# Kernel optimization log

Hardware: AMD Instinct MI355X
Metric: run time of the kernel (lower is better)

Reference implementation:

```python
import jax, jax.numpy as jnp
import numpy as np

EPS = 1e-12  # F.normalize eps

def _l2norm(x, axis=-1):
    n = jnp.sqrt(jnp.sum(x * x, axis=axis, keepdims=True))
    return x / jnp.maximum(n, EPS)

def setup_inputs() -> dict:
    key = jax.random.key(0)
    k1, k2, k3, k4 = jax.random.split(key, 4)
    B, S, L, E, H = 16, 4096, 512, 1024, 1024
    return {
        'input_data': jax.random.normal(k1, (B, S, H), dtype=jnp.float32),
        'label_repr': jax.random.normal(k2, (B, L, E), dtype=jnp.float32),
        'W_proj': jax.random.normal(k3, (H, E), dtype=jnp.float32) * (1.0 / np.sqrt(E)),
        'padding_mask': jax.random.randint(k4, (B, S), 0, 2, dtype=jnp.int32),
    }

def reference(input_data, label_repr, W_proj, padding_mask):
    # project labels: [B, L, E] @ [E, H] -> [B, L, H]
    lab = jnp.einsum('ble,he->blh', label_repr, W_proj)
    x_n = _l2norm(input_data, axis=-1)        # [B, S, H]
    lab_n = _l2norm(lab, axis=-1)             # [B, L, H] (== normalize dim=1 after transpose)
    G = jnp.einsum('bsh,blh->bsl', x_n, lab_n)  # cosine scores [B, S, L]
    mask = (padding_mask == 0)[:, :, None]    # True where padded
    G = jnp.where(mask, -jnp.inf, G)
    softmax_G = jax.nn.softmax(G, axis=1)     # softmax over sequence axis
    output = jnp.einsum('bsl,bsh->blh', softmax_G, x_n)  # [B, L, H]
    return (output, softmax_G)
```

## Files before the change

kernel.cpp:

```cpp
#include <hip/hip_runtime.h>
#include <hip/hip_bf16.h>
#include <cmath>

#define B_DIM 16
#define S_DIM 4096
#define L_DIM 512
#define E_DIM 1024
#define H_DIM 1024

typedef __bf16 bf16;
typedef __attribute__((ext_vector_type(8))) __bf16 bf16x8;
typedef __attribute__((ext_vector_type(4))) __bf16 bf16x4;
typedef __attribute__((ext_vector_type(4))) float f32x4;
typedef __attribute__((ext_vector_type(8))) unsigned short u16x8;

__device__ __forceinline__ void gload_lds16(const void* g, void* l) {
  __builtin_amdgcn_global_load_lds((const __attribute__((address_space(1))) void*)g,
                                   (__attribute__((address_space(3))) void*)l,
                                   16, 0, 0);
}

#define SWZ(o) ((o) ^ ((((o) >> 9) & 1) << 5))

__global__ void k_cast(const float* __restrict__ in, bf16* __restrict__ out, int n4) {
  int stride = gridDim.x * blockDim.x;
  for (int i = blockIdx.x * blockDim.x + threadIdx.x; i < n4; i += stride) {
    float4 v = reinterpret_cast<const float4*>(in)[i];
    bf16x4 o = { (bf16)v.x, (bf16)v.y, (bf16)v.z, (bf16)v.w };
    reinterpret_cast<bf16x4*>(out)[i] = o;
  }
}

__global__ __launch_bounds__(256) void k_rownorm_f32(const float* __restrict__ in,
                                                     bf16* __restrict__ out, int nrows) {
  const int wave = (blockIdx.x * 256 + threadIdx.x) >> 6;
  const int lane = threadIdx.x & 63;
  const int nw = (gridDim.x * 256) >> 6;
  for (int r = wave; r < nrows; r += nw) {
    const float4* src = reinterpret_cast<const float4*>(in + (size_t)r * 1024);
    float4 v[4];
    float ss = 0.f;
#pragma unroll
    for (int j = 0; j < 4; ++j) {
      v[j] = src[lane + j * 64];
      ss += v[j].x * v[j].x + v[j].y * v[j].y + v[j].z * v[j].z + v[j].w * v[j].w;
    }
#pragma unroll
    for (int off = 32; off; off >>= 1) ss += __shfl_xor(ss, off);
    const float inv = 1.0f / fmaxf(sqrtf(ss), 1e-12f);
    bf16x4* dst = reinterpret_cast<bf16x4*>(out + (size_t)r * 1024);
#pragma unroll
    for (int j = 0; j < 4; ++j) {
      bf16x4 o = { (bf16)(v[j].x * inv), (bf16)(v[j].y * inv), (bf16)(v[j].z * inv),
                   (bf16)(v[j].w * inv) };
      dst[lane + j * 64] = o;
    }
  }
}

__global__ __launch_bounds__(256) void k_rownorm_add(const float* __restrict__ P,
                                                     bf16* __restrict__ out, int nrows) {
  const int wave = (blockIdx.x * 256 + threadIdx.x) >> 6;
  const int lane = threadIdx.x & 63;
  const int nw = (gridDim.x * 256) >> 6;
  for (int r = wave; r < nrows; r += nw) {
    const int b = r >> 9, l = r & 511;
    const float* p0 = P + ((size_t)b * 1024 + l) * 1024;
    const float4* s0 = reinterpret_cast<const float4*>(p0);
    const float4* s1 = reinterpret_cast<const float4*>(p0 + 524288);
    float4 v[4];
    float ss = 0.f;
#pragma unroll
    for (int j = 0; j < 4; ++j) {
      float4 a = s0[lane + j * 64], c = s1[lane + j * 64];
      v[j] = make_float4(a.x + c.x, a.y + c.y, a.z + c.z, a.w + c.w);
      ss += v[j].x * v[j].x + v[j].y * v[j].y + v[j].z * v[j].z + v[j].w * v[j].w;
    }
#pragma unroll
    for (int off = 32; off; off >>= 1) ss += __shfl_xor(ss, off);
    const float inv = 1.0f / fmaxf(sqrtf(ss), 1e-12f);
    bf16x4* dst = reinterpret_cast<bf16x4*>(out + (size_t)r * 1024);
#pragma unroll
    for (int j = 0; j < 4; ++j) {
      bf16x4 o = { (bf16)(v[j].x * inv), (bf16)(v[j].y * inv), (bf16)(v[j].z * inv),
                   (bf16)(v[j].w * inv) };
      dst[lane + j * 64] = o;
    }
  }
}

__global__ void k_addout(const float* __restrict__ P, float* __restrict__ out, int total4,
                         int LH4) {
  int stride = gridDim.x * blockDim.x;
  for (int i = blockIdx.x * blockDim.x + threadIdx.x; i < total4; i += stride) {
    int b = i / LH4, rem = i - b * LH4;
    const float4* p0 = reinterpret_cast<const float4*>(P) + (size_t)b * 2 * LH4 + rem;
    float4 a = p0[0], c = p0[LH4];
    reinterpret_cast<float4*>(out)[i] = make_float4(a.x + c.x, a.y + c.y, a.z + c.z, a.w + c.w);
  }
}

__global__ __launch_bounds__(256) void k_transpose(const bf16* __restrict__ in,
                                                   bf16* __restrict__ out, int R, int C) {
  __shared__ unsigned short tile[64][72];
  const int r0 = blockIdx.x * 64, c0 = blockIdx.y * 64;
  const size_t boff = (size_t)blockIdx.z * (size_t)R * C;
  const unsigned short* src = (const unsigned short*)in + boff;
  unsigned short* dst = (unsigned short*)out + boff;
  const int t = threadIdx.x;
#pragma unroll
  for (int p = 0; p < 2; ++p) {
    int r = p * 32 + (t >> 3);
    int c = (t & 7) * 8;
    u16x8 v = *reinterpret_cast<const u16x8*>(src + (size_t)(r0 + r) * C + c0 + c);
#pragma unroll
    for (int j = 0; j < 8; ++j) tile[r][c + j] = v[j];
  }
  __syncthreads();
#pragma unroll
  for (int p = 0; p < 2; ++p) {
    int cc = p * 32 + (t >> 3);
    int rr = (t & 7) * 8;
    u16x8 o;
#pragma unroll
    for (int j = 0; j < 8; ++j) o[j] = tile[rr + j][cc];
    *reinterpret_cast<u16x8*>(dst + (size_t)(c0 + cc) * R + r0 + rr) = o;
  }
}

template <int MODE, int KSPLIT>
__global__ __launch_bounds__(512, 2) void k_gemm8(
    const bf16* __restrict__ Aall, const bf16* __restrict__ Ball, void* __restrict__ Call,
    const int N, const int ldk, const int Klen, const size_t sA, const size_t sB,
    const size_t sC, const int lg_nbx, const int* __restrict__ mask,
    float2* __restrict__ part) {
  extern __shared__ char lds[];
  const int bid = blockIdx.x, ntot = gridDim.x;
  const int wg = (bid & 7) * (ntot >> 3) + (bid >> 3);
  const int by = wg & 1;
  const int tmp2 = wg >> 1;
  const int bx = tmp2 & ((1 << lg_nbx) - 1);
  const int z = tmp2 >> lg_nbx;
  const int b = z / KSPLIT, ks = z - b * KSPLIT;
  const int koff = ks * Klen;
  const int t = threadIdx.x, wid = t >> 6, lane = t & 63;
  const int wm = wid >> 2, wn = wid & 3;
  const int lane_r = lane & 15;
  const int lane_k = (lane >> 4) * 16;
  const int row0 = by * 256, col0 = bx * 256;
  const bf16* srcA = Aall + (size_t)b * sA + (size_t)row0 * ldk + koff;
  const bf16* srcB = Ball + (size_t)b * sB + (size_t)col0 * ldk + koff;
  const int NKT = Klen >> 6;

  int s_r[2], s_ce[2];
#pragma unroll
  for (int li = 0; li < 2; ++li) {
    int o = li * 8192 + t * 16;
    int so = SWZ(o);
    s_r[li] = so >> 7;
    s_ce[li] = (so & 127) >> 1;
  }

  f32x4 acc[8][4];
#pragma unroll
  for (int i = 0; i < 8; ++i)
#pragma unroll
    for (int j = 0; j < 4; ++j) acc[i][j] = (f32x4){0.f, 0.f, 0.f, 0.f};

  bf16x8 aq[4][2], b0[2][2], b1[2][2];

  auto STAGE = [&](int c, int isB, int h, const bf16* src, int kt_idx) {
#pragma unroll
    for (int li = 0; li < 2; ++li) {
      const bf16* g = src + (size_t)(h * 128 + s_r[li]) * ldk + (kt_idx * 64 + s_ce[li]);
      char* d = lds + c * 65536 + isB * 32768 + h * 16384 + li * 8192 + wid * 1024;
      gload_lds16(g, d);
    }
  };
  auto LDA = [&](int c, int mh) {
#pragma unroll
    for (int mi = 0; mi < 4; ++mi)
#pragma unroll
      for (int kk = 0; kk < 2; ++kk) {
        int rl = (mh * 4 + mi) * 16 + lane_r;
        int o = rl * 128 + lane_k + kk * 64;
        aq[mi][kk] =
            *reinterpret_cast<const bf16x8*>(lds + c * 65536 + wm * 16384 + SWZ(o));
      }
  };
  auto LDB = [&](int c, int nh, bf16x8(&bq)[2][2]) {
#pragma unroll
    for (int ni = 0; ni < 2; ++ni)
#pragma unroll
      for (int kk = 0; kk < 2; ++kk) {
        int rl = (wn & 1) * 64 + (nh * 2 + ni) * 16 + lane_r;
        int o = rl * 128 + lane_k + kk * 64;
        bq[ni][kk] = *reinterpret_cast<const bf16x8*>(lds + c * 65536 + 32768 +
                                                      (wn >> 1) * 16384 + SWZ(o));
      }
  };
  auto MMA = [&](int mh, int nh, bf16x8(&bq)[2][2]) {
#pragma unroll
    for (int mi = 0; mi < 4; ++mi)
#pragma unroll
      for (int ni = 0; ni < 2; ++ni)
#pragma unroll
        for (int kk = 0; kk < 2; ++kk)
          acc[mh * 4 + mi][nh * 2 + ni] = __builtin_amdgcn_mfma_f32_16x16x32_bf16(
              aq[mi][kk], bq[ni][kk], acc[mh * 4 + mi][nh * 2 + ni], 0, 0, 0);
  };

#define GS_BEGIN                                        \
  __builtin_amdgcn_s_barrier();                         \
  asm volatile("s_waitcnt lgkmcnt(0)" ::: "memory");    \
  __builtin_amdgcn_sched_barrier(0);                    \
  __builtin_amdgcn_s_setprio(1);
#define GS_END                                          \
  __builtin_amdgcn_s_setprio(0);                        \
  __builtin_amdgcn_s_barrier();

  STAGE(0, 0, 0, srcA, 0);
  STAGE(0, 1, 0, srcB, 0);
  STAGE(0, 0, 1, srcA, 0);
  STAGE(0, 1, 1, srcB, 0);
  STAGE(1, 0, 0, srcA, 1);
  STAGE(1, 1, 0, srcB, 1);
  STAGE(1, 0, 1, srcA, 1);
  asm volatile("s_waitcnt vmcnt(6)" ::: "memory");
  __builtin_amdgcn_s_barrier();

#pragma unroll 1
  for (int kt = 0; kt < NKT; kt += 2) {
    const bool s2 = kt + 2 < NKT, s3 = kt + 3 < NKT;
    LDA(0, 0);
    LDB(0, 0, b0);
    STAGE(1, 1, 1, srcB, kt + 1);
    GS_BEGIN; MMA(0, 0, b0); GS_END;
    LDB(0, 1, b1);
    GS_BEGIN; MMA(0, 1, b1); GS_END;
    LDA(0, 1);
    if (s2) STAGE(0, 1, 0, srcB, kt + 2);
    GS_BEGIN; MMA(1, 1, b1); GS_END;
    if (s2) {
      STAGE(0, 0, 0, srcA, kt + 2);
      asm volatile("s_waitcnt vmcnt(4)" ::: "memory");
    } else {
      asm volatile("s_waitcnt vmcnt(0)" ::: "memory");
    }
    GS_BEGIN; MMA(1, 0, b0); GS_END;
    LDA(1, 0);
    LDB(1, 0, b0);
    if (s2) STAGE(0, 1, 1, srcB, kt + 2);
    GS_BEGIN; MMA(0, 0, b0); GS_END;
    LDB(1, 1, b1);
    if (s2) STAGE(0, 0, 1, srcA, kt + 2);
    GS_BEGIN; MMA(0, 1, b1); GS_END;
    LDA(1, 1);
    if (s3) STAGE(1, 1, 0, srcB, kt + 3);
    GS_BEGIN; MMA(1, 1, b1); GS_END;
    if (s3) {
      STAGE(1, 0, 0, srcA, kt + 3);
      STAGE(1, 0, 1, srcA, kt + 3);
      asm volatile("s_waitcnt vmcnt(6)" ::: "memory");
    } else {
      asm volatile("s_waitcnt vmcnt(0)" ::: "memory");
    }
    GS_BEGIN; MMA(1, 0, b0); GS_END;
  }
#undef GS_BEGIN
#undef GS_END

  const int rb = row0 + wm * 128 + (lane >> 4) * 4;
  const int cb = col0 + wn * 64 + lane_r;
  if (MODE == 2) {
    bf16* C = (bf16*)Call + (size_t)z * sC;
#pragma unroll
    for (int mf = 0; mf < 8; ++mf)
#pragma unroll
      for (int nf = 0; nf < 4; ++nf)
#pragma unroll
        for (int r = 0; r < 4; ++r)
          C[(size_t)(rb + mf * 16 + r) * N + cb + nf * 16] = (bf16)acc[mf][nf][r];
    bool vld[4];
#pragma unroll
    for (int nf = 0; nf < 4; ++nf)
      vld[nf] = mask[(size_t)b * N + col0 + wn * 64 + nf * 16 + lane_r] != 0;
    float2* smb = reinterpret_cast<float2*>(lds);
#pragma unroll
    for (int mf = 0; mf < 8; ++mf)
#pragma unroll
      for (int r = 0; r < 4; ++r) {
        float m = -INFINITY;
#pragma unroll
        for (int nf = 0; nf < 4; ++nf)
          if (vld[nf]) m = fmaxf(m, acc[mf][nf][r]);
#pragma unroll
        for (int off = 1; off < 16; off <<= 1) m = fmaxf(m, __shfl_xor(m, off));
        float zz = 0.f;
#pragma unroll
        for (int nf = 0; nf < 4; ++nf)
          if (vld[nf]) zz += __expf(acc[mf][nf][r] - m);
#pragma unroll
        for (int off = 1; off < 16; off <<= 1) zz += __shfl_xor(zz, off);
        if (lane_r == 0)
          smb[(wm * 128 + mf * 16 + (lane >> 4) * 4 + r) * 4 + wn] = make_float2(m, zz);
      }
    __syncthreads();
    if (t < 256) {
      float2 p0 = smb[t * 4 + 0], p1 = smb[t * 4 + 1], p2 = smb[t * 4 + 2],
             p3 = smb[t * 4 + 3];
      float M = fmaxf(fmaxf(p0.x, p1.x), fmaxf(p2.x, p3.x));
      float Z = 0.f;
      if (M != -INFINITY)
        Z = p0.y * __expf(p0.x - M) + p1.y * __expf(p1.x - M) + p2.y * __expf(p2.x - M) +
            p3.y * __expf(p3.x - M);
      part[((size_t)b * L_DIM + row0 + t) * 16 + bx] = make_float2(M, Z);
    }
  } else {
    float* C = (float*)Call + (size_t)z * sC;
#pragma unroll
    for (int mf = 0; mf < 8; ++mf)
#pragma unroll
      for (int nf = 0; nf < 4; ++nf)
#pragma unroll
        for (int r = 0; r < 4; ++r)
          C[(size_t)(rb + mf * 16 + r) * N + cb + nf * 16] = acc[mf][nf][r];
  }
}

__global__ void k_sm_comb(const float2* __restrict__ part, float2* __restrict__ mz, int n) {
  int id = blockIdx.x * blockDim.x + threadIdx.x;
  if (id >= n) return;
  float2 p[16];
  float M = -INFINITY;
#pragma unroll
  for (int q = 0; q < 16; ++q) {
    p[q] = part[(size_t)id * 16 + q];
    M = fmaxf(M, p[q].x);
  }
  float Z = 0.f;
  if (M != -INFINITY) {
#pragma unroll
    for (int q = 0; q < 16; ++q)
      if (p[q].x != -INFINITY) Z += p[q].y * __expf(p[q].x - M);
  }
  float rZ = (Z > 0.f) ? 1.0f / Z : 0.f;
  mz[id] = make_float2(M, rZ);
}

__global__ __launch_bounds__(256) void k_sm_write(bf16* __restrict__ GT,
                                                  const int* __restrict__ mask,
                                                  const float2* __restrict__ mz,
                                                  float* __restrict__ out1) {
  __shared__ float tile[64][65];
  const int b = blockIdx.z, lt = blockIdx.y, sc = blockIdx.x;
  const int t = threadIdx.x, w = t >> 6, lane = t & 63;
  const int s_base = sc * 512;
  for (int st = 0; st < 8; ++st) {
    const int s_tile = s_base + st * 64;
    const bool v = (mask[(size_t)b * S_DIM + s_tile + lane] != 0);
#pragma unroll
    for (int i = 0; i < 16; ++i) {
      const int l = lt * 64 + w * 16 + i;
      const float2 mzv = mz[(size_t)b * L_DIM + l];
      bf16* rp = GT + ((size_t)b * L_DIM + l) * S_DIM + s_tile + lane;
      const float g = (float)*rp;
      const float p = (v && mzv.x != -INFINITY) ? __expf(g - mzv.x) * mzv.y : 0.f;
      *rp = (bf16)p;
      tile[lane][w * 16 + i] = p;
    }
    __syncthreads();
#pragma unroll
    for (int q = 0; q < 16; ++q) {
      const int s_local = q * 4 + w;
      out1[((size_t)b * S_DIM + s_tile + s_local) * L_DIM + lt * 64 + lane] =
          tile[s_local][lane];
    }
    __syncthreads();
  }
}

extern "C" void kernel_launch(void* const* d_in, const int* in_sizes, int n_in, void* d_out,
                              int out_size, void* d_ws, size_t ws_size, hipStream_t stream) {
  const float* input_data = (const float*)d_in[0];
  const float* label_repr = (const float*)d_in[1];
  const float* W_proj = (const float*)d_in[2];
  const int* padding = (const int*)d_in[3];
  float* out0 = (float*)d_out;
  float* out1 = out0 + (size_t)B_DIM * L_DIM * H_DIM;

  char* ws = (char*)d_ws;
  bf16* xn = (bf16*)(ws + 0);
  bf16* xnT = (bf16*)(ws + 134217728);
  bf16* labb = (bf16*)(ws + 268435456);
  bf16* Wb = (bf16*)(ws + 285212672);
  bf16* lab = (bf16*)(ws + 287309824);
  bf16* GT = (bf16*)(ws + 304087040);
  float2* part = (float2*)(ws + 371195904);
  float2* mz = (float2*)(ws + 372244480);
  float* Pk2 = (float*)(ws + 304087040);
  float* Pk5 = (float*)(ws + 0);

  (void)hipFuncSetAttribute((const void*)k_gemm8<0, 2>,
                            hipFuncAttributeMaxDynamicSharedMemorySize, 131072);
  (void)hipFuncSetAttribute((const void*)k_gemm8<2, 1>,
                            hipFuncAttributeMaxDynamicSharedMemorySize, 131072);

  k_cast<<<2048, 256, 0, stream>>>(label_repr, labb, (B_DIM * L_DIM * E_DIM) / 4);
  k_cast<<<512, 256, 0, stream>>>(W_proj, Wb, (H_DIM * E_DIM) / 4);
  k_rownorm_f32<<<2048, 256, 0, stream>>>(input_data, xn, B_DIM * S_DIM);
  k_transpose<<<dim3(S_DIM / 64, H_DIM / 64, B_DIM), 256, 0, stream>>>(xn, xnT, S_DIM, H_DIM);
  k_gemm8<0, 2><<<256, 512, 131072, stream>>>(labb, Wb, Pk2, H_DIM, E_DIM, 512,
                                              (size_t)L_DIM * E_DIM, 0,
                                              (size_t)L_DIM * H_DIM, 2, nullptr, nullptr);
  k_rownorm_add<<<512, 256, 0, stream>>>(Pk2, lab, B_DIM * L_DIM);
  k_gemm8<2, 1><<<512, 512, 131072, stream>>>(lab, xn, GT, S_DIM, H_DIM, H_DIM,
                                              (size_t)L_DIM * H_DIM, (size_t)S_DIM * H_DIM,
                                              (size_t)L_DIM * S_DIM, 4, padding, part);
  k_sm_comb<<<(B_DIM * L_DIM + 255) / 256, 256, 0, stream>>>(part, mz, B_DIM * L_DIM);
  k_sm_write<<<dim3(8, 8, B_DIM), 256, 0, stream>>>(GT, padding, mz, out1);
  k_gemm8<0, 2><<<256, 512, 131072, stream>>>(GT, xnT, Pk5, H_DIM, S_DIM, 2048,
                                              (size_t)L_DIM * S_DIM, (size_t)H_DIM * S_DIM,
                                              (size_t)L_DIM * H_DIM, 2, nullptr, nullptr);
  k_addout<<<2048, 256, 0, stream>>>(Pk5, out0, (B_DIM * L_DIM * H_DIM) / 4,
                                     (L_DIM * H_DIM) / 4);
}
```

Baseline: 460.6 us.

## Fuse input row-normalization with transpose and drop split-K for label projection

A new kernel loads 32 input rows per block, L2-normalizes them, and writes both the row-major bf16 copy and the transposed copy through an LDS tile. This replaces the separate normalize and transpose kernels and removes one bf16 round trip through global memory. The label projection GEMM now runs without split-K (128 blocks over the full K), so the plain row-norm kernel can replace the add-and-normalize kernel. The trade-off is fewer blocks in that GEMM and a high-register fused kernel holding 32 float4 values per thread.

Result: slower. 531.0 us (+15.3%).

```diff
diff --git a/kernel.cpp b/kernel.cpp
--- a/kernel.cpp
+++ b/kernel.cpp
@@ -28,6 +28,54 @@
     float4 v = reinterpret_cast<const float4*>(in)[i];
     bf16x4 o = { (bf16)v.x, (bf16)v.y, (bf16)v.z, (bf16)v.w };
     reinterpret_cast<bf16x4*>(out)[i] = o;
+  }
+}
+
+__global__ __launch_bounds__(256, 2) void k_normtrans(const float* __restrict__ in,
+                                                      bf16* __restrict__ xn,
+                                                      bf16* __restrict__ xnT) {
+  __shared__ unsigned short tile[32][1032];
+  __shared__ float ssw[4][32];
+  const int b = blockIdx.y;
+  const int s0 = blockIdx.x * 32;
+  const int t = threadIdx.x, w = t >> 6, lane = t & 63;
+  const float* src = in + ((size_t)b * S_DIM + s0) * 1024;
+  float4 v[32];
+#pragma unroll
+  for (int r = 0; r < 32; ++r) {
+    v[r] = reinterpret_cast<const float4*>(src + (size_t)r * 1024)[t];
+    float ss = v[r].x * v[r].x + v[r].y * v[r].y + v[r].z * v[r].z + v[r].w * v[r].w;
+#pragma unroll
+    for (int off = 32; off; off >>= 1) ss += __shfl_xor(ss, off);
+    if (lane == 0) ssw[w][r] = ss;
+  }
+  __syncthreads();
+#pragma unroll
+  for (int r = 0; r < 32; ++r) {
+    const float tot = ssw[0][r] + ssw[1][r] + ssw[2][r] + ssw[3][r];
+    const float inv = 1.0f / fmaxf(sqrtf(tot), 1e-12f);
+    bf16x4 o = { (bf16)(v[r].x * inv), (bf16)(v[r].y * inv), (bf16)(v[r].z * inv),
+                 (bf16)(v[r].w * inv) };
+    reinterpret_cast<bf16x4*>(xn + ((size_t)b * S_DIM + s0 + r) * 1024)[t] = o;
+    *reinterpret_cast<bf16x4*>(&tile[r][t * 4]) = o;
+  }
+  __syncthreads();
+#pragma unroll
+  for (int i = 0; i < 4; ++i) {
+    const int h = i * 256 + t;
+    u16x8 o0, o1, o2, o3;
+#pragma unroll
+    for (int j = 0; j < 8; ++j) {
+      o0[j] = tile[j][h];
+      o1[j] = tile[8 + j][h];
+      o2[j] = tile[16 + j][h];
+      o3[j] = tile[24 + j][h];
+    }
+    unsigned short* dst = (unsigned short*)xnT + ((size_t)b * H_DIM + h) * S_DIM + s0;
+    *reinterpret_cast<u16x8*>(dst) = o0;
+    *reinterpret_cast<u16x8*>(dst + 8) = o1;
+    *reinterpret_cast<u16x8*>(dst + 16) = o2;
+    *reinterpret_cast<u16x8*>(dst + 24) = o3;
   }
 }
 
@@ -58,37 +106,6 @@
   }
 }
 
-__global__ __launch_bounds__(256) void k_rownorm_add(const float* __restrict__ P,
-                                                     bf16* __restrict__ out, int nrows) {
-  const int wave = (blockIdx.x * 256 + threadIdx.x) >> 6;
-  const int lane = threadIdx.x & 63;
-  const int nw = (gridDim.x * 256) >> 6;
-  for (int r = wave; r < nrows; r += nw) {
-    const int b = r >> 9, l = r & 511;
-    const float* p0 = P + ((size_t)b * 1024 + l) * 1024;
-    const float4* s0 = reinterpret_cast<const float4*>(p0);
-    const float4* s1 = reinterpret_cast<const float4*>(p0 + 524288);
-    float4 v[4];
-    float ss = 0.f;
-#pragma unroll
-    for (int j = 0; j < 4; ++j) {
-      float4 a = s0[lane + j * 64], c = s1[lane + j * 64];
-      v[j] = make_float4(a.x + c.x, a.y + c.y, a.z + c.z, a.w + c.w);
-      ss += v[j].x * v[j].x + v[j].y * v[j].y + v[j].z * v[j].z + v[j].w * v[j].w;
-    }
-#pragma unroll
-    for (int off = 32; off; off >>= 1) ss += __shfl_xor(ss, off);
-    const float inv = 1.0f / fmaxf(sqrtf(ss), 1e-12f);
-    bf16x4* dst = reinterpret_cast<bf16x4*>(out + (size_t)r * 1024);
-#pragma unroll
-    for (int j = 0; j < 4; ++j) {
-      bf16x4 o = { (bf16)(v[j].x * inv), (bf16)(v[j].y * inv), (bf16)(v[j].z * inv),
-                   (bf16)(v[j].w * inv) };
-      dst[lane + j * 64] = o;
-    }
-  }
-}
-
 __global__ void k_addout(const float* __restrict__ P, float* __restrict__ out, int total4,
                          int LH4) {
   int stride = gridDim.x * blockDim.x;
@@ -97,34 +114,6 @@
     const float4* p0 = reinterpret_cast<const float4*>(P) + (size_t)b * 2 * LH4 + rem;
     float4 a = p0[0], c = p0[LH4];
     reinterpret_cast<float4*>(out)[i] = make_float4(a.x + c.x, a.y + c.y, a.z + c.z, a.w + c.w);
-  }
-}
-
-__global__ __launch_bounds__(256) void k_transpose(const bf16* __restrict__ in,
-                                                   bf16* __restrict__ out, int R, int C) {
-  __shared__ unsigned short tile[64][72];
-  const int r0 = blockIdx.x * 64, c0 = blockIdx.y * 64;
-  const size_t boff = (size_t)blockIdx.z * (size_t)R * C;
-  const unsigned short* src = (const unsigned short*)in + boff;
-  unsigned short* dst = (unsigned short*)out + boff;
-  const int t = threadIdx.x;
-#pragma unroll
-  for (int p = 0; p < 2; ++p) {
-    int r = p * 32 + (t >> 3);
-    int c = (t & 7) * 8;
-    u16x8 v = *reinterpret_cast<const u16x8*>(src + (size_t)(r0 + r) * C + c0 + c);
-#pragma unroll
-    for (int j = 0; j < 8; ++j) tile[r][c + j] = v[j];
-  }
-  __syncthreads();
-#pragma unroll
-  for (int p = 0; p < 2; ++p) {
-    int cc = p * 32 + (t >> 3);
-    int rr = (t & 7) * 8;
-    u16x8 o;
-#pragma unroll
-    for (int j = 0; j < 8; ++j) o[j] = tile[rr + j][cc];
-    *reinterpret_cast<u16x8*>(dst + (size_t)(c0 + cc) * R + r0 + rr) = o;
   }
 }
 
@@ -401,6 +390,8 @@
   float* Pk2 = (float*)(ws + 304087040);
   float* Pk5 = (float*)(ws + 0);
 
+  (void)hipFuncSetAttribute((const void*)k_gemm8<0, 1>,
+                            hipFuncAttributeMaxDynamicSharedMemorySize, 131072);
   (void)hipFuncSetAttribute((const void*)k_gemm8<0, 2>,
                             hipFuncAttributeMaxDynamicSharedMemorySize, 131072);
   (void)hipFuncSetAttribute((const void*)k_gemm8<2, 1>,
@@ -408,12 +399,11 @@
 
   k_cast<<<2048, 256, 0, stream>>>(label_repr, labb, (B_DIM * L_DIM * E_DIM) / 4);
   k_cast<<<512, 256, 0, stream>>>(W_proj, Wb, (H_DIM * E_DIM) / 4);
-  k_rownorm_f32<<<2048, 256, 0, stream>>>(input_data, xn, B_DIM * S_DIM);
-  k_transpose<<<dim3(S_DIM / 64, H_DIM / 64, B_DIM), 256, 0, stream>>>(xn, xnT, S_DIM, H_DIM);
-  k_gemm8<0, 2><<<256, 512, 131072, stream>>>(labb, Wb, Pk2, H_DIM, E_DIM, 512,
+  k_normtrans<<<dim3(S_DIM / 32, B_DIM), 256, 0, stream>>>(input_data, xn, xnT);
+  k_gemm8<0, 1><<<128, 512, 131072, stream>>>(labb, Wb, Pk2, H_DIM, E_DIM, E_DIM,
                                               (size_t)L_DIM * E_DIM, 0,
                                               (size_t)L_DIM * H_DIM, 2, nullptr, nullptr);
-  k_rownorm_add<<<512, 256, 0, stream>>>(Pk2, lab, B_DIM * L_DIM);
+  k_rownorm_f32<<<512, 256, 0, stream>>>(Pk2, lab, B_DIM * L_DIM);
   k_gemm8<2, 1><<<512, 512, 131072, stream>>>(lab, xn, GT, S_DIM, H_DIM, H_DIM,
                                               (size_t)L_DIM * H_DIM, (size_t)S_DIM * H_DIM,
                                               (size_t)L_DIM * S_DIM, 4, padding, part);
```
